# Kernel tuning notes

Hardware: AMD Instinct MI355X
Metric: run time of the kernel (lower is better)

## Reference

```python
import jax, jax.numpy as jnp
import numpy as np

B, IN_DIM, OUT_DIM, N = 8, 128, 128, 256
BN_EPS = 1e-5


def setup_inputs() -> dict:
    key = jax.random.key(0)
    ks = jax.random.split(key, 6)
    A = jax.random.normal(ks[0], (B, IN_DIM, N), dtype=jnp.float32)
    ini_p = float(np.sqrt(3.0 / OUT_DIM / IN_DIM))
    ini_qk = float(np.sqrt(1.0 / OUT_DIM / IN_DIM))
    P1 = jax.random.uniform(ks[1], (OUT_DIM, IN_DIM), minval=-ini_p, maxval=ini_p, dtype=jnp.float32)
    P2 = jax.random.uniform(ks[2], (OUT_DIM, IN_DIM), minval=-ini_p, maxval=ini_p, dtype=jnp.float32)
    q = jax.random.uniform(ks[3], (OUT_DIM, IN_DIM), minval=-ini_qk, maxval=ini_qk, dtype=jnp.float32)
    k = jax.random.uniform(ks[4], (OUT_DIM, IN_DIM), minval=-ini_qk, maxval=ini_qk, dtype=jnp.float32)
    gamma = jnp.ones((OUT_DIM,), dtype=jnp.float32)
    beta = jnp.zeros((OUT_DIM,), dtype=jnp.float32)
    return {"A": A, "P1": P1, "P2": P2, "q": q, "k": k,
            "gamma": gamma, "beta": beta,
            "permutation_size1": N, "BATCH_SIZE": B}


def reference(A, P1, P2, q, k, gamma, beta, permutation_size1, BATCH_SIZE):
    # A: [B, in_dim, n]; params [out_dim, in_dim]
    A1 = jnp.einsum('oi,bin->bon', P1, A)            # [B, C, n]
    Q = jnp.einsum('oi,bin->bon', q, A)              # [B, C, n]
    K = jnp.einsum('oi,bin->bon', k, A)              # [B, C, n]
    # Rank-1 outer product per (b, c): Alpha[b,c,i,j] = Q[b,c,i] * K[b,c,j]
    Alpha = Q[..., :, None] * K[..., None, :]        # [B, C, n, n]
    row_norm = jnp.linalg.norm(Alpha, axis=3, keepdims=True)  # [B, C, n, 1]
    Alpha_norm = jnp.abs(Alpha) / row_norm
    V = jnp.einsum('oi,bin->bon', P2, A)             # [B, C, n]
    Y = jnp.einsum('bcij,bcj->bci', Alpha_norm, V)   # [B, C, n]
    out = A1 + V + 0.1 * Y
    out = jax.nn.relu(out)
    # BatchNorm1d (training mode): normalize per channel over (B, n)
    mean = out.mean(axis=(0, 2), keepdims=True)
    var = out.var(axis=(0, 2), keepdims=True)
    out = (out - mean) * jax.lax.rsqrt(var + BN_EPS)
    out = out * gamma[None, :, None] + beta[None, :, None]
    return out
```

## Files before the change

kernel.cpp:

```cpp
#include <hip/hip_runtime.h>
#include <math.h>

#define BB   8
#define IND  128
#define OUTD 128
#define NN   256
#define NQ   64
#define BN_EPS 1e-5f

__global__ __launch_bounds__(128) void k1_proj(
    const float* __restrict__ A,
    const float* __restrict__ P1,
    const float* __restrict__ P2,
    const float* __restrict__ kw,
    float* __restrict__ pbuf,
    float* __restrict__ bnp)
{
    const int c = blockIdx.x;
    const int b = blockIdx.y;
    const int x = threadIdx.x;
    const int z = threadIdx.y;

    const float4* __restrict__ A4 = (const float4*)A + (size_t)b * IND * NQ;
    const float* __restrict__ w1 = P1 + c * IND;
    const float* __restrict__ w2 = P2 + c * IND;
    const float* __restrict__ w3 = kw + c * IND;

    float a1[4] = {0.f, 0.f, 0.f, 0.f};
    float vv[4] = {0.f, 0.f, 0.f, 0.f};
    float kv[4] = {0.f, 0.f, 0.f, 0.f};

    const int ibase = z * 64;
    #pragma unroll
    for (int blk = 0; blk < 8; ++blk) {
        float4 cur[8];
        #pragma unroll
        for (int j = 0; j < 8; ++j)
            cur[j] = A4[(ibase + blk * 8 + j) * NQ + x];
        #pragma unroll
        for (int j = 0; j < 8; ++j) {
            const int i = ibase + blk * 8 + j;
            const float wa = w1[i], wb = w2[i], wc = w3[i];
            a1[0] = fmaf(wa, cur[j].x, a1[0]); a1[1] = fmaf(wa, cur[j].y, a1[1]);
            a1[2] = fmaf(wa, cur[j].z, a1[2]); a1[3] = fmaf(wa, cur[j].w, a1[3]);
            vv[0] = fmaf(wb, cur[j].x, vv[0]); vv[1] = fmaf(wb, cur[j].y, vv[1]);
            vv[2] = fmaf(wb, cur[j].z, vv[2]); vv[3] = fmaf(wb, cur[j].w, vv[3]);
            kv[0] = fmaf(wc, cur[j].x, kv[0]); kv[1] = fmaf(wc, cur[j].y, kv[1]);
            kv[2] = fmaf(wc, cur[j].z, kv[2]); kv[3] = fmaf(wc, cur[j].w, kv[3]);
        }
    }

    __shared__ float part[64][13];
    if (z == 1) {
        #pragma unroll
        for (int j = 0; j < 4; ++j) {
            part[x][j]     = a1[j];
            part[x][4 + j] = vv[j];
            part[x][8 + j] = kv[j];
        }
    }
    __syncthreads();
    if (z != 0) return;

    #pragma unroll
    for (int j = 0; j < 4; ++j) {
        a1[j] += part[x][j];
        vv[j] += part[x][4 + j];
        kv[j] += part[x][8 + j];
    }

    float s2 = 0.f, sv = 0.f;
    #pragma unroll
    for (int j = 0; j < 4; ++j) {
        s2 = fmaf(kv[j], kv[j], s2);
        sv = fmaf(fabsf(kv[j]), vv[j], sv);
    }
    #pragma unroll
    for (int off = 32; off >= 1; off >>= 1) {
        s2 += __shfl_xor(s2, off, 64);
        sv += __shfl_xor(sv, off, 64);
    }
    const float y = sv / sqrtf(s2);

    float p[4];
    float bnsum = 0.f, bnsq = 0.f;
    #pragma unroll
    for (int j = 0; j < 4; ++j) {
        float t = a1[j] + vv[j] + 0.1f * y;
        t = fmaxf(t, 0.f);
        p[j] = t;
        bnsum += t;
        bnsq  = fmaf(t, t, bnsq);
    }
    #pragma unroll
    for (int off = 32; off >= 1; off >>= 1) {
        bnsum += __shfl_xor(bnsum, off, 64);
        bnsq  += __shfl_xor(bnsq,  off, 64);
    }

    float4* __restrict__ p4 = (float4*)pbuf;
    p4[((size_t)b * OUTD + c) * NQ + x] = make_float4(p[0], p[1], p[2], p[3]);
    if (x == 0) {
        bnp[c * BB + b]             = bnsum;
        bnp[OUTD * BB + c * BB + b] = bnsq;
    }
}

__global__ __launch_bounds__(64) void k2_bn(
    const float* __restrict__ pbuf,
    const float* __restrict__ bnp,
    const float* __restrict__ gamma,
    const float* __restrict__ beta,
    float* __restrict__ out)
{
    const int c = blockIdx.x;
    const int b = blockIdx.y;
    const int x = threadIdx.x;

    float tsum = 0.f, tsq = 0.f;
    #pragma unroll
    for (int w = 0; w < BB; ++w) {
        tsum += bnp[c * BB + w];
        tsq  += bnp[OUTD * BB + c * BB + w];
    }
    const float inv   = 1.f / (float)(BB * NN);
    const float mean  = tsum * inv;
    const float var   = tsq * inv - mean * mean;
    const float scale = gamma[c] * rsqrtf(var + BN_EPS);
    const float shift = beta[c] - mean * scale;

    const float4* __restrict__ p4 = (const float4*)pbuf;
    float4* __restrict__ out4 = (float4*)out;
    const size_t idx = ((size_t)b * OUTD + c) * NQ + x;
    const float4 p = p4[idx];
    out4[idx] = make_float4(fmaf(p.x, scale, shift), fmaf(p.y, scale, shift),
                            fmaf(p.z, scale, shift), fmaf(p.w, scale, shift));
}

extern "C" void kernel_launch(void* const* d_in, const int* in_sizes, int n_in,
                              void* d_out, int out_size, void* d_ws, size_t ws_size,
                              hipStream_t stream) {
    const float* A     = (const float*)d_in[0];
    const float* P1    = (const float*)d_in[1];
    const float* P2    = (const float*)d_in[2];
    const float* kw    = (const float*)d_in[4];
    const float* gamma = (const float*)d_in[5];
    const float* beta  = (const float*)d_in[6];
    float* out = (float*)d_out;

    float* pbuf = (float*)d_ws;
    float* bnp  = (float*)((char*)d_ws + (size_t)BB * OUTD * NN * sizeof(float));

    dim3 g(OUTD, BB);
    k1_proj<<<g, dim3(64, 2), 0, stream>>>(A, P1, P2, kw, pbuf, bnp);
    k2_bn<<<g, 64, 0, stream>>>(pbuf, bnp, gamma, beta, out);
}
```

Measured before the change: 78.89 us.

## Compute two output channels per block and split input dim across four waves

```diff
diff --git a/kernel.cpp b/kernel.cpp
--- a/kernel.cpp
+++ b/kernel.cpp
@@ -7,8 +7,11 @@
 #define NN   256
 #define NQ   64
 #define BN_EPS 1e-5f
+#define ZW   4
+#define ISL  (IND/ZW)
+#define PST  25
 
-__global__ __launch_bounds__(128) void k1_proj(
+__global__ __launch_bounds__(64 * ZW) void k1_proj(
     const float* __restrict__ A,
     const float* __restrict__ P1,
     const float* __restrict__ P2,
@@ -16,23 +19,28 @@
     float* __restrict__ pbuf,
     float* __restrict__ bnp)
 {
-    const int c = blockIdx.x;
-    const int b = blockIdx.y;
-    const int x = threadIdx.x;
-    const int z = threadIdx.y;
+    const int cg = blockIdx.x;
+    const int b  = blockIdx.y;
+    const int x  = threadIdx.x;
+    const int z  = threadIdx.y;
+    const int c0 = cg * 2;
+    const int c1 = c0 + 1;
 
     const float4* __restrict__ A4 = (const float4*)A + (size_t)b * IND * NQ;
-    const float* __restrict__ w1 = P1 + c * IND;
-    const float* __restrict__ w2 = P2 + c * IND;
-    const float* __restrict__ w3 = kw + c * IND;
+    const float* __restrict__ w1a = P1 + c0 * IND;
+    const float* __restrict__ w1b = P1 + c1 * IND;
+    const float* __restrict__ w2a = P2 + c0 * IND;
+    const float* __restrict__ w2b = P2 + c1 * IND;
+    const float* __restrict__ w3a = kw + c0 * IND;
+    const float* __restrict__ w3b = kw + c1 * IND;
 
-    float a1[4] = {0.f, 0.f, 0.f, 0.f};
-    float vv[4] = {0.f, 0.f, 0.f, 0.f};
-    float kv[4] = {0.f, 0.f, 0.f, 0.f};
+    float a1[2][4] = {{0.f,0.f,0.f,0.f},{0.f,0.f,0.f,0.f}};
+    float vv[2][4] = {{0.f,0.f,0.f,0.f},{0.f,0.f,0.f,0.f}};
+    float kv[2][4] = {{0.f,0.f,0.f,0.f},{0.f,0.f,0.f,0.f}};
 
-    const int ibase = z * 64;
+    const int ibase = z * ISL;
     #pragma unroll
-    for (int blk = 0; blk < 8; ++blk) {
+    for (int blk = 0; blk < ISL / 8; ++blk) {
         float4 cur[8];
         #pragma unroll
         for (int j = 0; j < 8; ++j)
@@ -40,69 +48,101 @@
         #pragma unroll
         for (int j = 0; j < 8; ++j) {
             const int i = ibase + blk * 8 + j;
-            const float wa = w1[i], wb = w2[i], wc = w3[i];
-            a1[0] = fmaf(wa, cur[j].x, a1[0]); a1[1] = fmaf(wa, cur[j].y, a1[1]);
-            a1[2] = fmaf(wa, cur[j].z, a1[2]); a1[3] = fmaf(wa, cur[j].w, a1[3]);
-            vv[0] = fmaf(wb, cur[j].x, vv[0]); vv[1] = fmaf(wb, cur[j].y, vv[1]);
-            vv[2] = fmaf(wb, cur[j].z, vv[2]); vv[3] = fmaf(wb, cur[j].w, vv[3]);
-            kv[0] = fmaf(wc, cur[j].x, kv[0]); kv[1] = fmaf(wc, cur[j].y, kv[1]);
-            kv[2] = fmaf(wc, cur[j].z, kv[2]); kv[3] = fmaf(wc, cur[j].w, kv[3]);
+            const float wa0 = w1a[i], wa1 = w1b[i];
+            const float wb0 = w2a[i], wb1 = w2b[i];
+            const float wc0 = w3a[i], wc1 = w3b[i];
+            a1[0][0]=fmaf(wa0,cur[j].x,a1[0][0]); a1[0][1]=fmaf(wa0,cur[j].y,a1[0][1]);
+            a1[0][2]=fmaf(wa0,cur[j].z,a1[0][2]); a1[0][3]=fmaf(wa0,cur[j].w,a1[0][3]);
+            a1[1][0]=fmaf(wa1,cur[j].x,a1[1][0]); a1[1][1]=fmaf(wa1,cur[j].y,a1[1][1]);
+            a1[1][2]=fmaf(wa1,cur[j].z,a1[1][2]); a1[1][3]=fmaf(wa1,cur[j].w,a1[1][3]);
+            vv[0][0]=fmaf(wb0,cur[j].x,vv[0][0]); vv[0][1]=fmaf(wb0,cur[j].y,vv[0][1]);
+            vv[0][2]=fmaf(wb0,cur[j].z,vv[0][2]); vv[0][3]=fmaf(wb0,cur[j].w,vv[0][3]);
+            vv[1][0]=fmaf(wb1,cur[j].x,vv[1][0]); vv[1][1]=fmaf(wb1,cur[j].y,vv[1][1]);
+            vv[1][2]=fmaf(wb1,cur[j].z,vv[1][2]); vv[1][3]=fmaf(wb1,cur[j].w,vv[1][3]);
+            kv[0][0]=fmaf(wc0,cur[j].x,kv[0][0]); kv[0][1]=fmaf(wc0,cur[j].y,kv[0][1]);
+            kv[0][2]=fmaf(wc0,cur[j].z,kv[0][2]); kv[0][3]=fmaf(wc0,cur[j].w,kv[0][3]);
+            kv[1][0]=fmaf(wc1,cur[j].x,kv[1][0]); kv[1][1]=fmaf(wc1,cur[j].y,kv[1][1]);
+            kv[1][2]=fmaf(wc1,cur[j].z,kv[1][2]); kv[1][3]=fmaf(wc1,cur[j].w,kv[1][3]);
         }
     }
 
-    __shared__ float part[64][13];
-    if (z == 1) {
+    __shared__ float part[ZW - 1][64][PST];
+    if (z > 0) {
+        float* dst = part[z - 1][x];
         #pragma unroll
-        for (int j = 0; j < 4; ++j) {
-            part[x][j]     = a1[j];
-            part[x][4 + j] = vv[j];
-            part[x][8 + j] = kv[j];
-        }
+        for (int ch = 0; ch < 2; ++ch)
+            #pragma unroll
+            for (int j = 0; j < 4; ++j) {
+                dst[ch * 12 + j]     = a1[ch][j];
+                dst[ch * 12 + 4 + j] = vv[ch][j];
+                dst[ch * 12 + 8 + j] = kv[ch][j];
+            }
     }
     __syncthreads();
     if (z != 0) return;
 
     #pragma unroll
-    for (int j = 0; j < 4; ++j) {
-        a1[j] += part[x][j];
-        vv[j] += part[x][4 + j];
-        kv[j] += part[x][8 + j];
+    for (int zz = 0; zz < ZW - 1; ++zz) {
+        const float* src = part[zz][x];
+        #pragma unroll
+        for (int ch = 0; ch < 2; ++ch)
+            #pragma unroll
+            for (int j = 0; j < 4; ++j) {
+                a1[ch][j] += src[ch * 12 + j];
+                vv[ch][j] += src[ch * 12 + 4 + j];
+                kv[ch][j] += src[ch * 12 + 8 + j];
+            }
     }
 
-    float s2 = 0.f, sv = 0.f;
+    float s2[2], sv[2];
     #pragma unroll
-    for (int j = 0; j < 4; ++j) {
-        s2 = fmaf(kv[j], kv[j], s2);
-        sv = fmaf(fabsf(kv[j]), vv[j], sv);
+    for (int ch = 0; ch < 2; ++ch) {
+        s2[ch] = 0.f; sv[ch] = 0.f;
+        #pragma unroll
+        for (int j = 0; j < 4; ++j) {
+            s2[ch] = fmaf(kv[ch][j], kv[ch][j], s2[ch]);
+            sv[ch] = fmaf(fabsf(kv[ch][j]), vv[ch][j], sv[ch]);
+        }
     }
     #pragma unroll
     for (int off = 32; off >= 1; off >>= 1) {
-        s2 += __shfl_xor(s2, off, 64);
-        sv += __shfl_xor(sv, off, 64);
+        s2[0] += __shfl_xor(s2[0], off, 64);
+        sv[0] += __shfl_xor(sv[0], off, 64);
+        s2[1] += __shfl_xor(s2[1], off, 64);
+        sv[1] += __shfl_xor(sv[1], off, 64);
     }
-    const float y = sv / sqrtf(s2);
 
-    float p[4];
-    float bnsum = 0.f, bnsq = 0.f;
+    float p[2][4];
+    float bnsum[2], bnsq[2];
     #pragma unroll
-    for (int j = 0; j < 4; ++j) {
-        float t = a1[j] + vv[j] + 0.1f * y;
-        t = fmaxf(t, 0.f);
-        p[j] = t;
-        bnsum += t;
-        bnsq  = fmaf(t, t, bnsq);
+    for (int ch = 0; ch < 2; ++ch) {
+        const float y = sv[ch] / sqrtf(s2[ch]);
+        bnsum[ch] = 0.f; bnsq[ch] = 0.f;
+        #pragma unroll
+        for (int j = 0; j < 4; ++j) {
+            float t = a1[ch][j] + vv[ch][j] + 0.1f * y;
+            t = fmaxf(t, 0.f);
+            p[ch][j] = t;
+            bnsum[ch] += t;
+            bnsq[ch]  = fmaf(t, t, bnsq[ch]);
+        }
     }
     #pragma unroll
     for (int off = 32; off >= 1; off >>= 1) {
-        bnsum += __shfl_xor(bnsum, off, 64);
-        bnsq  += __shfl_xor(bnsq,  off, 64);
+        bnsum[0] += __shfl_xor(bnsum[0], off, 64);
+        bnsq[0]  += __shfl_xor(bnsq[0],  off, 64);
+        bnsum[1] += __shfl_xor(bnsum[1], off, 64);
+        bnsq[1]  += __shfl_xor(bnsq[1],  off, 64);
     }
 
     float4* __restrict__ p4 = (float4*)pbuf;
-    p4[((size_t)b * OUTD + c) * NQ + x] = make_float4(p[0], p[1], p[2], p[3]);
+    p4[((size_t)b * OUTD + c0) * NQ + x] = make_float4(p[0][0], p[0][1], p[0][2], p[0][3]);
+    p4[((size_t)b * OUTD + c1) * NQ + x] = make_float4(p[1][0], p[1][1], p[1][2], p[1][3]);
     if (x == 0) {
-        bnp[c * BB + b]             = bnsum;
-        bnp[OUTD * BB + c * BB + b] = bnsq;
+        bnp[c0 * BB + b]             = bnsum[0];
+        bnp[c1 * BB + b]             = bnsum[1];
+        bnp[OUTD * BB + c0 * BB + b] = bnsq[0];
+        bnp[OUTD * BB + c1 * BB + b] = bnsq[1];
     }
 }
 
@@ -151,7 +191,6 @@
     float* pbuf = (float*)d_ws;
     float* bnp  = (float*)((char*)d_ws + (size_t)BB * OUTD * NN * sizeof(float));
 
-    dim3 g(OUTD, BB);
-    k1_proj<<<g, dim3(64, 2), 0, stream>>>(A, P1, P2, kw, pbuf, bnp);
-    k2_bn<<<g, 64, 0, stream>>>(pbuf, bnp, gamma, beta, out);
+    k1_proj<<<dim3(OUTD / 2, BB), dim3(64, ZW), 0, stream>>>(A, P1, P2, kw, pbuf, bnp);
+    k2_bn<<<dim3(OUTD, BB), 64, 0, stream>>>(pbuf, bnp, gamma, beta, out);
 }
```

After: 79.66 us. No clear change (+1.0%).
